# Optimization experiments

Measured on AMD Instinct MI355X. Metric: run time of the kernel, lower is better.

The kernel has to match this reference:

```python
import jax, jax.numpy as jnp
import numpy as np

N_NODES = 100000
N_EDGES = 3200000
IN_DIM = 4
HID = 128
OUT_DIM = 4


def setup_inputs() -> dict:
    key = jax.random.key(0)
    ks = jax.random.split(key, 16)
    x = jax.random.normal(ks[0], (N_NODES, IN_DIM), dtype=jnp.float32)
    edge_index = jax.random.randint(ks[1], (2, N_EDGES), 0, N_NODES, dtype=jnp.int32)
    hidden_mask = jax.random.randint(ks[2], (N_NODES,), 0, 2) > 0
    def glorot(k, shape):
        fan_in, fan_out = shape[0], shape[1]
        s = jnp.sqrt(6.0 / (fan_in + fan_out))
        return jax.random.uniform(k, shape, jnp.float32, -s, s)
    return {
        "x": x,
        "edge_index": edge_index,
        "hidden_mask": hidden_mask,
        "W0": glorot(ks[3], (IN_DIM, HID)), "b0": jnp.zeros((HID,), jnp.float32),
        "res_W": glorot(ks[4], (IN_DIM, HID)), "res_b": jnp.zeros((HID,), jnp.float32),
        "W1": glorot(ks[5], (HID, HID)), "b1": jnp.zeros((HID,), jnp.float32),
        "W2": glorot(ks[6], (HID, HID)), "b2": jnp.zeros((HID,), jnp.float32),
        "fc_W": glorot(ks[7], (HID, OUT_DIM)), "fc_b": jnp.zeros((OUT_DIM,), jnp.float32),
    }


def _gcn_norm(edge_index, num_nodes):
    # add self loops, compute symmetric normalization (PyG GCNConv default)
    loop = jnp.arange(num_nodes, dtype=edge_index.dtype)
    src = jnp.concatenate([edge_index[0], loop])
    dst = jnp.concatenate([edge_index[1], loop])
    deg = jax.ops.segment_sum(jnp.ones_like(dst, dtype=jnp.float32), dst,
                              num_segments=num_nodes)
    dis = jnp.where(deg > 0, jax.lax.rsqrt(deg), 0.0)  # deg^{-1/2}, inf -> 0
    norm = dis[src] * dis[dst]  # [E + N]
    return src, dst, norm


def _gcn_conv(h, W, b, src, dst, norm, num_nodes):
    h = h @ W                       # [N, out]
    msg = h[src] * norm[:, None]    # gather + scale, [E+N, out]
    agg = jax.ops.segment_sum(msg, dst, num_segments=num_nodes)
    return agg + b


def reference(x, edge_index, hidden_mask, W0, b0, res_W, res_b, W1, b1, W2, b2, fc_W, fc_b):
    n = x.shape[0]
    src, dst, norm = _gcn_norm(edge_index, n)
    # mask input features (mask broadcast over 4 feature cols)
    h = jnp.where(hidden_mask[:, None], x, 0.0)
    # layer 0: in_dim != hidden -> linear residual
    out0 = _gcn_conv(h, W0, b0, src, dst, norm, n)
    h = jax.nn.relu(out0 + (h @ res_W + res_b))
    # layers 1,2: identity residual
    h = jax.nn.relu(_gcn_conv(h, W1, b1, src, dst, norm, n) + h)
    h = jax.nn.relu(_gcn_conv(h, W2, b2, src, dst, norm, n) + h)
    x_out = h @ fc_W + fc_b
    return (x_out, hidden_mask)
```

## Files before the change

kernel.cpp:

```cpp
#include <hip/hip_runtime.h>
#include <hip/hip_bf16.h>
#include <stdint.h>

#define HID 128
#define NPART 8
#define NCHUNK 256
#define MCHUNK 4096
#define LBITS 9
#define SBITS 22
#define NCH 8

typedef float f2 __attribute__((ext_vector_type(2)));

__global__ void detect_mask_kernel(const unsigned char* __restrict__ p, int nbytes,
                                   int nfloat, int* __restrict__ flags) {
  int stride = blockDim.x * gridDim.x;
  for (int i = blockIdx.x * blockDim.x + threadIdx.x; i < nbytes; i += stride) {
    if ((i & 3) && p[i] != 0) { atomicOr(&flags[0], 1); break; }
  }
  const float* fp = (const float*)p;
  for (int i = blockIdx.x * blockDim.x + threadIdx.x; i < nfloat; i += stride) {
    float f = fp[i];
    if (!(f == 0.0f || f == 1.0f)) { atomicOr(&flags[1], 1); break; }
  }
}

__global__ void expand_mask_h0(const void* __restrict__ maskp, const float4* __restrict__ x4,
                               const int* __restrict__ flags, const float* __restrict__ dis,
                               float* __restrict__ maskout, float* __restrict__ cvec,
                               float4* __restrict__ h0s, int N) {
  int i = blockIdx.x * blockDim.x + threadIdx.x;
  if (i >= N) return;
  float m;
  if (flags[0] == 0)      m = (((const int*)maskp)[i] != 0) ? 1.f : 0.f;
  else if (flags[1] == 0) m = (((const float*)maskp)[i] != 0.f) ? 1.f : 0.f;
  else                    m = (((const unsigned char*)maskp)[i] != 0) ? 1.f : 0.f;
  maskout[i] = m;
  float4 xv = x4[i];
  float4 h0 = make_float4(m * xv.x, m * xv.y, m * xv.z, m * xv.w);
  float* cv = cvec + (size_t)i * 8;
  cv[4] = h0.x; cv[5] = h0.y; cv[6] = h0.z; cv[7] = h0.w;
  float d = dis[i];
  h0s[i] = make_float4(d * h0.x, d * h0.y, d * h0.z, d * h0.w);
}

__global__ void init_gcur_kernel(int* __restrict__ gcur, int n, int CAPB) {
  int i = blockIdx.x * blockDim.x + threadIdx.x;
  if (i < n) gcur[i] = i * CAPB;
}

__global__ void radixA_kernel(const int* __restrict__ src, const int* __restrict__ dst,
                              int* __restrict__ gcur, uint32_t* __restrict__ bdata,
                              int nbin, int CAPB, int E) {
  __shared__ uint32_t sv[MCHUNK];
  __shared__ uint16_t sb[MCHUNK];
  __shared__ int bcnt[1024], boff[1024], gbase[1024];
  __shared__ int wsum[4];
  int t = threadIdx.x;
  int base = blockIdx.x * MCHUNK;
  int m = E - base; if (m > MCHUNK) m = MCHUNK;
  for (int i = t; i < 1024; i += 256) bcnt[i] = 0;
  __syncthreads();
  uint32_t pk[16]; short bn[16];
#pragma unroll
  for (int j = 0; j < 16; j++) {
    int i = base + t + j * 256;
    if (i < base + m) {
      int d = __builtin_nontemporal_load(&dst[i]);
      int s = __builtin_nontemporal_load(&src[i]);
      int b = d >> LBITS;
      pk[j] = ((uint32_t)(d & ((1 << LBITS) - 1)) << SBITS) | (uint32_t)s;
      bn[j] = (short)b;
      atomicAdd(&bcnt[b], 1);
    } else bn[j] = -1;
  }
  __syncthreads();
  {
    int lane = t & 63, w = t >> 6, i0 = t * 4;
    int v0 = bcnt[i0], v1 = bcnt[i0 + 1], v2 = bcnt[i0 + 2], v3 = bcnt[i0 + 3];
    int ts = v0 + v1 + v2 + v3, sc = ts;
    for (int d = 1; d < 64; d <<= 1) { int x = __shfl_up(sc, d, 64); if (lane >= d) sc += x; }
    if (lane == 63) wsum[w] = sc;
    __syncthreads();
    int wo = 0;
    for (int k = 0; k < w; k++) wo += wsum[k];
    int excl = wo + sc - ts;
    boff[i0] = excl; boff[i0 + 1] = excl + v0;
    boff[i0 + 2] = excl + v0 + v1; boff[i0 + 3] = excl + v0 + v1 + v2;
  }
  __syncthreads();
  for (int i = t; i < nbin; i += 256) {
    int c = bcnt[i];
    gbase[i] = c ? atomicAdd(&gcur[i], c) : 0;
  }
  __syncthreads();
  for (int i = t; i < nbin; i += 256) bcnt[i] = boff[i];
  __syncthreads();
#pragma unroll
  for (int j = 0; j < 16; j++) {
    if (bn[j] >= 0) {
      int p = atomicAdd(&bcnt[bn[j]], 1);
      sv[p] = pk[j];
      sb[p] = (uint16_t)bn[j];
    }
  }
  __syncthreads();
  for (int i = t; i < m; i += 256) {
    int b = sb[i];
    int gp = gbase[b] + (i - boff[b]);
    if (gp < (b + 1) * CAPB) bdata[gp] = sv[i];
  }
}

__global__ void bucket_meta_kernel(const int* __restrict__ gcur, int* __restrict__ bstart,
                                   int nbin, int CAPB) {
  __shared__ int wsum[4];
  int t = threadIdx.x, lane = t & 63, w = t >> 6, i0 = t * 4;
  int v[4];
#pragma unroll
  for (int q = 0; q < 4; q++) {
    int i = i0 + q;
    int c = 0;
    if (i < nbin) {
      c = gcur[i] - i * CAPB;
      if (c > CAPB) c = CAPB;
    }
    v[q] = c;
  }
  int ts = v[0] + v[1] + v[2] + v[3], sc = ts;
  for (int d = 1; d < 64; d <<= 1) { int x = __shfl_up(sc, d, 64); if (lane >= d) sc += x; }
  if (lane == 63) wsum[w] = sc;
  __syncthreads();
  int wo = 0;
  for (int k = 0; k < w; k++) wo += wsum[k];
  int excl = wo + sc - ts;
  int e[4] = {excl, excl + v[0], excl + v[0] + v[1], excl + v[0] + v[1] + v[2]};
#pragma unroll
  for (int q = 0; q < 4; q++)
    if (i0 + q < nbin) bstart[i0 + q] = e[q];
  if (t == 255) bstart[nbin] = wo + sc;
}

__global__ void radixB_kernel(const uint32_t* __restrict__ bdata, const int* __restrict__ gcur,
                              const int* __restrict__ bstart, int CAPB,
                              int* __restrict__ off, float* __restrict__ dis,
                              float* __restrict__ rdis, int* __restrict__ csr,
                              int N, int E, int cshift) {
  __shared__ int cnt[4096], loff[4096];
  __shared__ int wsum[4];
  int b = blockIdx.x, t = threadIdx.x;
  int cb = gcur[b] - b * CAPB; if (cb > CAPB) cb = CAPB;
  int gb = bstart[b];
  const uint32_t* bd = bdata + (size_t)b * CAPB;
  for (int i = t; i < 4096; i += 256) cnt[i] = 0;
  __syncthreads();
  const uint32_t smask = (1u << SBITS) - 1;
  for (int i = t; i < cb; i += 256) {
    uint32_t v = bd[i];
    int ld = v >> SBITS;
    int src = (int)(v & smask);
    atomicAdd(&cnt[(ld << 3) | (src >> cshift)], 1);
  }
  __syncthreads();
  int lane = t & 63, w = t >> 6;
  int loc[16];
  int s = 0;
  int base16 = t * 16;
#pragma unroll
  for (int q = 0; q < 16; q++) { loc[q] = cnt[base16 + q]; s += loc[q]; }
  int sc = s;
  for (int d = 1; d < 64; d <<= 1) { int x = __shfl_up(sc, d, 64); if (lane >= d) sc += x; }
  if (lane == 63) wsum[w] = sc;
  __syncthreads();
  int wo = 0;
  for (int k = 0; k < w; k++) wo += wsum[k];
  int excl = wo + sc - s;
  {
    int run = excl;
#pragma unroll
    for (int q = 0; q < 16; q++) { loff[base16 + q] = run; run += loc[q]; }
  }
  int c0 = loc[0] + loc[1] + loc[2] + loc[3] + loc[4] + loc[5] + loc[6] + loc[7];
  int c1 = loc[8] + loc[9] + loc[10] + loc[11] + loc[12] + loc[13] + loc[14] + loc[15];
  int dst0 = b * (1 << LBITS) + 2 * t;
  if (dst0 < N) {
    off[dst0] = gb + excl;
    dis[dst0] = rsqrtf((float)c0 + 1.0f);
    rdis[dst0] = sqrtf((float)c0 + 1.0f);
  }
  if (dst0 + 1 < N) {
    off[dst0 + 1] = gb + excl + c0;
    dis[dst0 + 1] = rsqrtf((float)c1 + 1.0f);
    rdis[dst0 + 1] = sqrtf((float)c1 + 1.0f);
  }
  if (b == 0 && t == 0) off[N] = E;
  __syncthreads();
  for (int i = t; i < 4096; i += 256) cnt[i] = loff[i];
  __syncthreads();
  for (int i = t; i < cb; i += 256) {
    uint32_t v = bd[i];
    int ld = v >> SBITS;
    int src = (int)(v & smask);
    int p = atomicAdd(&cnt[(ld << 3) | (src >> cshift)], 1);
    csr[gb + p] = src;
  }
}

__global__ void scan1_kernel(const int* __restrict__ cnt, int* __restrict__ off,
                             int* __restrict__ bsum, float* __restrict__ dis, int N) {
  __shared__ int wsum[4];
  int t = threadIdx.x, lane = t & 63, w = t >> 6;
  int base = blockIdx.x * 1024 + t * 4;
  int v0 = (base + 0 < N) ? cnt[base + 0] : 0;
  int v1 = (base + 1 < N) ? cnt[base + 1] : 0;
  int v2 = (base + 2 < N) ? cnt[base + 2] : 0;
  int v3 = (base + 3 < N) ? cnt[base + 3] : 0;
  if (dis) {
    if (base + 0 < N) dis[base + 0] = rsqrtf((float)v0 + 1.0f);
    if (base + 1 < N) dis[base + 1] = rsqrtf((float)v1 + 1.0f);
    if (base + 2 < N) dis[base + 2] = rsqrtf((float)v2 + 1.0f);
    if (base + 3 < N) dis[base + 3] = rsqrtf((float)v3 + 1.0f);
  }
  int ts = v0 + v1 + v2 + v3;
  int sc = ts;
  for (int d = 1; d < 64; d <<= 1) {
    int x = __shfl_up(sc, d, 64);
    if (lane >= d) sc += x;
  }
  if (lane == 63) wsum[w] = sc;
  __syncthreads();
  int wo = 0;
  for (int i = 0; i < w; i++) wo += wsum[i];
  int excl = wo + sc - ts;
  if (base + 0 < N) off[base + 0] = excl;
  if (base + 1 < N) off[base + 1] = excl + v0;
  if (base + 2 < N) off[base + 2] = excl + v0 + v1;
  if (base + 3 < N) off[base + 3] = excl + v0 + v1 + v2;
  if (t == 255) bsum[blockIdx.x] = wo + sc;
}

__global__ void scan2_kernel(int* __restrict__ bsum, int nb) {
  if (threadIdx.x == 0 && blockIdx.x == 0) {
    int run = 0;
    for (int i = 0; i < nb; i++) { int v = bsum[i]; bsum[i] = run; run += v; }
  }
}

__global__ void scan3_kernel(int* __restrict__ off, const int* __restrict__ bsum,
                             int* __restrict__ cur, int N, int E) {
  int i = blockIdx.x * blockDim.x + threadIdx.x;
  if (i < N) {
    int o = off[i] + bsum[i >> 10];
    off[i] = o;
    if (cur) cur[i] = o;
  }
  if (i == 0) off[N] = E;
}

__global__ void hist_part_kernel(const int* __restrict__ dst, int* __restrict__ cnt,
                                 int E, int N) {
  int p = blockIdx.x & (NPART - 1);
  int chunk = blockIdx.x >> 3;
  int lo = (int)((long long)p * N / NPART);
  int hi = (int)((long long)(p + 1) * N / NPART);
  int stride = NCHUNK * 256;
  for (int e = chunk * 256 + threadIdx.x; e < E; e += stride) {
    int d = __builtin_nontemporal_load(&dst[e]);
    if (d >= lo && d < hi) atomicAdd(&cnt[d], 1);
  }
}

__global__ void fill_part_kernel(const int* __restrict__ src, const int* __restrict__ dst,
                                 int* __restrict__ cur, int* __restrict__ csr, int E, int N) {
  int p = blockIdx.x & (NPART - 1);
  int chunk = blockIdx.x >> 3;
  int lo = (int)((long long)p * N / NPART);
  int hi = (int)((long long)(p + 1) * N / NPART);
  int stride = NCHUNK * 256;
  for (int e = chunk * 256 + threadIdx.x; e < E; e += stride) {
    int d = __builtin_nontemporal_load(&dst[e]);
    if (d >= lo && d < hi) {
      int s = __builtin_nontemporal_load(&src[e]);
      int pos = atomicAdd(&cur[d], 1);
      csr[pos] = s;
    }
  }
}

__global__ void l0_agg_kernel(const float4* __restrict__ h0s, const float* __restrict__ dis,
                              const int* __restrict__ off, const int* __restrict__ csr,
                              float* __restrict__ cvec, int N) {
  int n = blockIdx.x * blockDim.x + threadIdx.x;
  if (n >= N) return;
  float4 a = h0s[n];
  int e0 = off[n], e1 = off[n + 1];
  int i = e0;
  for (; i < e1 && (i & 3); i++) {
    float4 v = h0s[csr[i]];
    a.x += v.x; a.y += v.y; a.z += v.z; a.w += v.w;
  }
  for (; i + 4 <= e1; i += 4) {
    int4 c = *(const int4*)&csr[i];
    float4 v0 = h0s[c.x], v1 = h0s[c.y], v2 = h0s[c.z], v3 = h0s[c.w];
    a.x += v0.x + v1.x + v2.x + v3.x;
    a.y += v0.y + v1.y + v2.y + v3.y;
    a.z += v0.z + v1.z + v2.z + v3.z;
    a.w += v0.w + v1.w + v2.w + v3.w;
  }
  for (; i < e1; i++) {
    float4 v = h0s[csr[i]];
    a.x += v.x; a.y += v.y; a.z += v.z; a.w += v.w;
  }
  float dn = dis[n];
  float* cv = cvec + (size_t)n * 8;
  cv[0] = dn * a.x; cv[1] = dn * a.y; cv[2] = dn * a.z; cv[3] = dn * a.w;
}

__global__ void l0_combine_kernel(const float* __restrict__ cvec, const float* __restrict__ W0,
                                  const float* __restrict__ b0, const float* __restrict__ resW,
                                  const float* __restrict__ resb, const float* __restrict__ dis,
                                  float* __restrict__ h1, __hip_bfloat16* __restrict__ hbout) {
  int idx = blockIdx.x * blockDim.x + threadIdx.x;
  int n = idx >> 7, c = idx & 127;
  const float* cv = cvec + (size_t)n * 8;
  float acc = b0[c] + resb[c];
#pragma unroll
  for (int k = 0; k < 4; k++) {
    acc += cv[k] * W0[k * HID + c];
    acc += cv[4 + k] * resW[k * HID + c];
  }
  float v = fmaxf(acc, 0.0f);
  if (h1) h1[idx] = v;
  if (hbout) hbout[idx] = __float2bfloat16(dis[n] * v);
}

#define ACC2(W) { f2 v; v.x = __uint_as_float((W) << 16); \
                  v.y = __uint_as_float((W) & 0xffff0000u); a += v; }
__global__ void __launch_bounds__(256, 8)
agg_hid_bf16_kernel(const uint32_t* __restrict__ hb, const float* __restrict__ dis,
                    const int* __restrict__ off, const int* __restrict__ csr,
                    float* __restrict__ out, int N) {
  int node = blockIdx.x * 4 + (threadIdx.x >> 6);
  int lane = threadIdx.x & 63;
  if (node >= N) return;
  uint32_t w = hb[(size_t)node * 64 + lane];
  f2 a;
  a.x = __uint_as_float(w << 16);
  a.y = __uint_as_float(w & 0xffff0000u);
  int e0 = __builtin_amdgcn_readfirstlane(off[node]);
  int e1 = __builtin_amdgcn_readfirstlane(off[node + 1]);
  int i = e0;
  for (; i < e1 && (i & 3); i++) {
    int s = __builtin_amdgcn_readfirstlane(csr[i]);
    uint32_t ww = hb[(size_t)s * 64 + lane];
    ACC2(ww)
  }
  for (; i + 8 <= e1; i += 8) {
    int4 c0 = *(const int4*)&csr[i];
    int4 c1 = *(const int4*)&csr[i + 4];
    int s0 = __builtin_amdgcn_readfirstlane(c0.x);
    int s1 = __builtin_amdgcn_readfirstlane(c0.y);
    int s2 = __builtin_amdgcn_readfirstlane(c0.z);
    int s3 = __builtin_amdgcn_readfirstlane(c0.w);
    int s4 = __builtin_amdgcn_readfirstlane(c1.x);
    int s5 = __builtin_amdgcn_readfirstlane(c1.y);
    int s6 = __builtin_amdgcn_readfirstlane(c1.z);
    int s7 = __builtin_amdgcn_readfirstlane(c1.w);
    uint32_t w0 = hb[(size_t)s0 * 64 + lane];
    uint32_t w1 = hb[(size_t)s1 * 64 + lane];
    uint32_t w2 = hb[(size_t)s2 * 64 + lane];
    uint32_t w3 = hb[(size_t)s3 * 64 + lane];
    uint32_t w4 = hb[(size_t)s4 * 64 + lane];
    uint32_t w5 = hb[(size_t)s5 * 64 + lane];
    uint32_t w6 = hb[(size_t)s6 * 64 + lane];
    uint32_t w7 = hb[(size_t)s7 * 64 + lane];
    ACC2(w0) ACC2(w1) ACC2(w2) ACC2(w3) ACC2(w4) ACC2(w5) ACC2(w6) ACC2(w7)
  }
  for (; i + 4 <= e1; i += 4) {
    int4 c = *(const int4*)&csr[i];
    int s0 = __builtin_amdgcn_readfirstlane(c.x);
    int s1 = __builtin_amdgcn_readfirstlane(c.y);
    int s2 = __builtin_amdgcn_readfirstlane(c.z);
    int s3 = __builtin_amdgcn_readfirstlane(c.w);
    uint32_t w0 = hb[(size_t)s0 * 64 + lane];
    uint32_t w1 = hb[(size_t)s1 * 64 + lane];
    uint32_t w2 = hb[(size_t)s2 * 64 + lane];
    uint32_t w3 = hb[(size_t)s3 * 64 + lane];
    ACC2(w0) ACC2(w1) ACC2(w2) ACC2(w3)
  }
  for (; i < e1; i++) {
    int s = __builtin_amdgcn_readfirstlane(csr[i]);
    uint32_t ww = hb[(size_t)s * 64 + lane];
    ACC2(ww)
  }
  float dn = dis[node];
  *(float2*)&out[(size_t)node * HID + 2 * lane] = make_float2(dn * a.x, dn * a.y);
}

__global__ void agg_hid_kernel(const float* __restrict__ h, const float* __restrict__ dis,
                               const int* __restrict__ off, const int* __restrict__ csr,
                               float* __restrict__ out, int N) {
  int node = blockIdx.x * 4 + (threadIdx.x >> 6);
  int lane = threadIdx.x & 63;
  if (node >= N) return;
  float dn = dis[node];
  const float* hrow = h + (size_t)node * HID;
  float a0 = dn * hrow[lane];
  float a1 = dn * hrow[lane + 64];
  int e0 = off[node], e1 = off[node + 1];
  for (int i = e0; i < e1; i++) {
    int s = csr[i];
    float d = dis[s];
    const float* hs = h + (size_t)s * HID;
    a0 += d * hs[lane];
    a1 += d * hs[lane + 64];
  }
  out[(size_t)node * HID + lane] = dn * a0;
  out[(size_t)node * HID + lane + 64] = dn * a1;
}

__global__ void gemm_resid_relu_kernel(const float* __restrict__ ag,
                                       const __hip_bfloat16* __restrict__ hbres,
                                       const float* __restrict__ rdis,
                                       const float* __restrict__ W, const float* __restrict__ b,
                                       const float* __restrict__ dis,
                                       __hip_bfloat16* __restrict__ hbout, int N) {
  __shared__ float ash[64 * HID];
  int t = threadIdx.x;
  int n0 = blockIdx.x * 64;
  for (int i = t; i < 64 * HID; i += 256) {
    int gn = n0 + (i >> 7);
    ash[i] = (gn < N) ? ag[(size_t)gn * HID + (i & 127)] : 0.0f;
  }
  __syncthreads();
  int tc = t & 31;
  int tn = t >> 5;
  float acc[8][4];
#pragma unroll
  for (int j = 0; j < 8; j++)
#pragma unroll
    for (int q = 0; q < 4; q++) acc[j][q] = 0.0f;

  for (int k = 0; k < HID; k += 4) {
    float4 w0 = *(const float4*)&W[(k + 0) * HID + tc * 4];
    float4 w1 = *(const float4*)&W[(k + 1) * HID + tc * 4];
    float4 w2 = *(const float4*)&W[(k + 2) * HID + tc * 4];
    float4 w3 = *(const float4*)&W[(k + 3) * HID + tc * 4];
#pragma unroll
    for (int j = 0; j < 8; j++) {
      float4 a = *(const float4*)&ash[(tn * 8 + j) * HID + k];
      acc[j][0] += a.x * w0.x + a.y * w1.x + a.z * w2.x + a.w * w3.x;
      acc[j][1] += a.x * w0.y + a.y * w1.y + a.z * w2.y + a.w * w3.y;
      acc[j][2] += a.x * w0.z + a.y * w1.z + a.z * w2.z + a.w * w3.z;
      acc[j][3] += a.x * w0.w + a.y * w1.w + a.z * w2.w + a.w * w3.w;
    }
  }
  float4 bv = *(const float4*)&b[tc * 4];
#pragma unroll
  for (int j = 0; j < 8; j++) {
    int gn = n0 + tn * 8 + j;
    if (gn < N) {
      float rd = rdis[gn];
      uint2 hu = *(const uint2*)&hbres[(size_t)gn * HID + tc * 4];
      float h0v = __uint_as_float(hu.x << 16) * rd;
      float h1v = __uint_as_float(hu.x & 0xffff0000u) * rd;
      float h2v = __uint_as_float(hu.y << 16) * rd;
      float h3v = __uint_as_float(hu.y & 0xffff0000u) * rd;
      float4 o;
      o.x = fmaxf(acc[j][0] + bv.x + h0v, 0.0f);
      o.y = fmaxf(acc[j][1] + bv.y + h1v, 0.0f);
      o.z = fmaxf(acc[j][2] + bv.z + h2v, 0.0f);
      o.w = fmaxf(acc[j][3] + bv.w + h3v, 0.0f);
      float dnn = dis[gn];
      __hip_bfloat162 p01 = __float22bfloat162_rn(make_float2(dnn * o.x, dnn * o.y));
      __hip_bfloat162 p23 = __float22bfloat162_rn(make_float2(dnn * o.z, dnn * o.w));
      *(__hip_bfloat162*)&hbout[(size_t)gn * HID + tc * 4] = p01;
      *(__hip_bfloat162*)&hbout[(size_t)gn * HID + tc * 4 + 2] = p23;
    }
  }
}

__global__ void gemm_resid_fc_kernel(const float* __restrict__ ag,
                                     const __hip_bfloat16* __restrict__ hbres,
                                     const float* __restrict__ rdis,
                                     const float* __restrict__ W, const float* __restrict__ b,
                                     const float* __restrict__ fcW, const float* __restrict__ fcb,
                                     float* __restrict__ out, int N) {
  __shared__ float ash[64 * HID];
  int t = threadIdx.x;
  int n0 = blockIdx.x * 64;
  for (int i = t; i < 64 * HID; i += 256) {
    int gn = n0 + (i >> 7);
    ash[i] = (gn < N) ? ag[(size_t)gn * HID + (i & 127)] : 0.0f;
  }
  __syncthreads();
  int tc = t & 31;
  int tn = t >> 5;
  float acc[8][4];
#pragma unroll
  for (int j = 0; j < 8; j++)
#pragma unroll
    for (int q = 0; q < 4; q++) acc[j][q] = 0.0f;

  for (int k = 0; k < HID; k += 4) {
    float4 w0 = *(const float4*)&W[(k + 0) * HID + tc * 4];
    float4 w1 = *(const float4*)&W[(k + 1) * HID + tc * 4];
    float4 w2 = *(const float4*)&W[(k + 2) * HID + tc * 4];
    float4 w3 = *(const float4*)&W[(k + 3) * HID + tc * 4];
#pragma unroll
    for (int j = 0; j < 8; j++) {
      float4 a = *(const float4*)&ash[(tn * 8 + j) * HID + k];
      acc[j][0] += a.x * w0.x + a.y * w1.x + a.z * w2.x + a.w * w3.x;
      acc[j][1] += a.x * w0.y + a.y * w1.y + a.z * w2.y + a.w * w3.y;
      acc[j][2] += a.x * w0.z + a.y * w1.z + a.z * w2.z + a.w * w3.z;
      acc[j][3] += a.x * w0.w + a.y * w1.w + a.z * w2.w + a.w * w3.w;
    }
  }
  float4 f0 = *(const float4*)&fcW[(tc * 4 + 0) * 4];
  float4 f1 = *(const float4*)&fcW[(tc * 4 + 1) * 4];
  float4 f2 = *(const float4*)&fcW[(tc * 4 + 2) * 4];
  float4 f3 = *(const float4*)&fcW[(tc * 4 + 3) * 4];
  float4 bv = *(const float4*)&b[tc * 4];
  float4 fb = *(const float4*)&fcb[0];
#pragma unroll
  for (int j = 0; j < 8; j++) {
    int gn = n0 + tn * 8 + j;
    float4 o = make_float4(0.f, 0.f, 0.f, 0.f);
    if (gn < N) {
      float rd = rdis[gn];
      uint2 hu = *(const uint2*)&hbres[(size_t)gn * HID + tc * 4];
      o.x = fmaxf(acc[j][0] + bv.x + __uint_as_float(hu.x << 16) * rd, 0.0f);
      o.y = fmaxf(acc[j][1] + bv.y + __uint_as_float(hu.x & 0xffff0000u) * rd, 0.0f);
      o.z = fmaxf(acc[j][2] + bv.z + __uint_as_float(hu.y << 16) * rd, 0.0f);
      o.w = fmaxf(acc[j][3] + bv.w + __uint_as_float(hu.y & 0xffff0000u) * rd, 0.0f);
    }
    float r0 = o.x * f0.x + o.y * f1.x + o.z * f2.x + o.w * f3.x;
    float r1 = o.x * f0.y + o.y * f1.y + o.z * f2.y + o.w * f3.y;
    float r2 = o.x * f0.z + o.y * f1.z + o.z * f2.z + o.w * f3.z;
    float r3 = o.x * f0.w + o.y * f1.w + o.z * f2.w + o.w * f3.w;
#pragma unroll
    for (int d = 1; d < 32; d <<= 1) {
      r0 += __shfl_xor(r0, d, 64);
      r1 += __shfl_xor(r1, d, 64);
      r2 += __shfl_xor(r2, d, 64);
      r3 += __shfl_xor(r3, d, 64);
    }
    if (tc == 0 && gn < N)
      *(float4*)&out[(size_t)gn * 4] =
          make_float4(r0 + fb.x, r1 + fb.y, r2 + fb.z, r3 + fb.w);
  }
}

__global__ void gemm_resid_relu_f32_kernel(const float* __restrict__ ag, float* __restrict__ hout,
                                           const float* __restrict__ hres,
                                           const float* __restrict__ W, const float* __restrict__ b,
                                           int N) {
  __shared__ float ash[64 * HID];
  int t = threadIdx.x;
  int n0 = blockIdx.x * 64;
  for (int i = t; i < 64 * HID; i += 256) {
    int gn = n0 + (i >> 7);
    ash[i] = (gn < N) ? ag[(size_t)gn * HID + (i & 127)] : 0.0f;
  }
  __syncthreads();
  int tc = t & 31;
  int tn = t >> 5;
  float acc[8][4];
#pragma unroll
  for (int j = 0; j < 8; j++)
#pragma unroll
    for (int q = 0; q < 4; q++) acc[j][q] = 0.0f;
  for (int k = 0; k < HID; k += 4) {
    float4 w0 = *(const float4*)&W[(k + 0) * HID + tc * 4];
    float4 w1 = *(const float4*)&W[(k + 1) * HID + tc * 4];
    float4 w2 = *(const float4*)&W[(k + 2) * HID + tc * 4];
    float4 w3 = *(const float4*)&W[(k + 3) * HID + tc * 4];
#pragma unroll
    for (int j = 0; j < 8; j++) {
      float4 a = *(const float4*)&ash[(tn * 8 + j) * HID + k];
      acc[j][0] += a.x * w0.x + a.y * w1.x + a.z * w2.x + a.w * w3.x;
      acc[j][1] += a.x * w0.y + a.y * w1.y + a.z * w2.y + a.w * w3.y;
      acc[j][2] += a.x * w0.z + a.y * w1.z + a.z * w2.z + a.w * w3.z;
      acc[j][3] += a.x * w0.w + a.y * w1.w + a.z * w2.w + a.w * w3.w;
    }
  }
  float4 bv = *(const float4*)&b[tc * 4];
#pragma unroll
  for (int j = 0; j < 8; j++) {
    int gn = n0 + tn * 8 + j;
    if (gn < N) {
      float4 hv = *(const float4*)&hres[(size_t)gn * HID + tc * 4];
      float4 o;
      o.x = fmaxf(acc[j][0] + bv.x + hv.x, 0.0f);
      o.y = fmaxf(acc[j][1] + bv.y + hv.y, 0.0f);
      o.z = fmaxf(acc[j][2] + bv.z + hv.z, 0.0f);
      o.w = fmaxf(acc[j][3] + bv.w + hv.w, 0.0f);
      *(float4*)&hout[(size_t)gn * HID + tc * 4] = o;
    }
  }
}

__global__ void gemm_resid_fc_f32_kernel(const float* __restrict__ ag,
                                         const float* __restrict__ hres,
                                         const float* __restrict__ W, const float* __restrict__ b,
                                         const float* __restrict__ fcW, const float* __restrict__ fcb,
                                         float* __restrict__ out, int N) {
  __shared__ float ash[64 * HID];
  int t = threadIdx.x;
  int n0 = blockIdx.x * 64;
  for (int i = t; i < 64 * HID; i += 256) {
    int gn = n0 + (i >> 7);
    ash[i] = (gn < N) ? ag[(size_t)gn * HID + (i & 127)] : 0.0f;
  }
  __syncthreads();
  int tc = t & 31;
  int tn = t >> 5;
  float acc[8][4];
#pragma unroll
  for (int j = 0; j < 8; j++)
#pragma unroll
    for (int q = 0; q < 4; q++) acc[j][q] = 0.0f;
  for (int k = 0; k < HID; k += 4) {
    float4 w0 = *(const float4*)&W[(k + 0) * HID + tc * 4];
    float4 w1 = *(const float4*)&W[(k + 1) * HID + tc * 4];
    float4 w2 = *(const float4*)&W[(k + 2) * HID + tc * 4];
    float4 w3 = *(const float4*)&W[(k + 3) * HID + tc * 4];
#pragma unroll
    for (int j = 0; j < 8; j++) {
      float4 a = *(const float4*)&ash[(tn * 8 + j) * HID + k];
      acc[j][0] += a.x * w0.x + a.y * w1.x + a.z * w2.x + a.w * w3.x;
      acc[j][1] += a.x * w0.y + a.y * w1.y + a.z * w2.y + a.w * w3.y;
      acc[j][2] += a.x * w0.z + a.y * w1.z + a.z * w2.z + a.w * w3.z;
      acc[j][3] += a.x * w0.w + a.y * w1.w + a.z * w2.w + a.w * w3.w;
    }
  }
  float4 f0 = *(const float4*)&fcW[(tc * 4 + 0) * 4];
  float4 f1 = *(const float4*)&fcW[(tc * 4 + 1) * 4];
  float4 f2 = *(const float4*)&fcW[(tc * 4 + 2) * 4];
  float4 f3 = *(const float4*)&fcW[(tc * 4 + 3) * 4];
  float4 bv = *(const float4*)&b[tc * 4];
  float4 fb = *(const float4*)&fcb[0];
#pragma unroll
  for (int j = 0; j < 8; j++) {
    int gn = n0 + tn * 8 + j;
    float4 o = make_float4(0.f, 0.f, 0.f, 0.f);
    if (gn < N) {
      float4 hv = *(const float4*)&hres[(size_t)gn * HID + tc * 4];
      o.x = fmaxf(acc[j][0] + bv.x + hv.x, 0.0f);
      o.y = fmaxf(acc[j][1] + bv.y + hv.y, 0.0f);
      o.z = fmaxf(acc[j][2] + bv.z + hv.z, 0.0f);
      o.w = fmaxf(acc[j][3] + bv.w + hv.w, 0.0f);
    }
    float r0 = o.x * f0.x + o.y * f1.x + o.z * f2.x + o.w * f3.x;
    float r1 = o.x * f0.y + o.y * f1.y + o.z * f2.y + o.w * f3.y;
    float r2 = o.x * f0.z + o.y * f1.z + o.z * f2.z + o.w * f3.z;
    float r3 = o.x * f0.w + o.y * f1.w + o.z * f2.w + o.w * f3.w;
#pragma unroll
    for (int d = 1; d < 32; d <<= 1) {
      r0 += __shfl_xor(r0, d, 64);
      r1 += __shfl_xor(r1, d, 64);
      r2 += __shfl_xor(r2, d, 64);
      r3 += __shfl_xor(r3, d, 64);
    }
    if (tc == 0 && gn < N)
      *(float4*)&out[(size_t)gn * 4] =
          make_float4(r0 + fb.x, r1 + fb.y, r2 + fb.z, r3 + fb.w);
  }
}

extern "C" void kernel_launch(void* const* d_in, const int* in_sizes, int n_in,
                              void* d_out, int out_size, void* d_ws, size_t ws_size,
                              hipStream_t stream) {
  const float* x = (const float*)d_in[0];
  const int* edge = (const int*)d_in[1];
  const void* maskp = d_in[2];
  const float* W0 = (const float*)d_in[3];
  const float* b0 = (const float*)d_in[4];
  const float* resW = (const float*)d_in[5];
  const float* resb = (const float*)d_in[6];
  const float* W1 = (const float*)d_in[7];
  const float* b1 = (const float*)d_in[8];
  const float* W2 = (const float*)d_in[9];
  const float* b2 = (const float*)d_in[10];
  const float* fcW = (const float*)d_in[11];
  const float* fcb = (const float*)d_in[12];
  float* out = (float*)d_out;

  int N = in_sizes[0] / 4;
  int E = in_sizes[1] / 2;
  const int* srcp = edge;
  const int* dstp = edge + E;

  char* ws = (char*)d_ws;
  size_t cursor = 0;
  auto alloc = [&](size_t bytes) { char* p = ws + cursor; cursor += (bytes + 511) & ~(size_t)511; return p; };
  int* flags = (int*)alloc(16);
  int* cnt = (int*)alloc((size_t)N * 4);
  float* dis = (float*)alloc((size_t)N * 4);
  float* rdis = (float*)alloc((size_t)N * 4);
  int* off = (int*)alloc((size_t)(N + 1) * 4);
  int* bsum = (int*)alloc(1024);
  int nbin = (N + (1 << LBITS) - 1) >> LBITS;
  int* gcur = (int*)alloc((size_t)(nbin + 1) * 4);
  int* bstart = (int*)alloc((size_t)(nbin + 1) * 4);
  int* csr = (int*)alloc((size_t)E * 4);
  float* h0s = (float*)alloc((size_t)N * 4 * 4);
  float* cvec = (float*)alloc((size_t)N * 8 * 4);
  float* buf0 = (float*)alloc((size_t)N * HID * 4);
  float* buf1 = (float*)alloc((size_t)N * HID * 4);
  size_t base_cursor = cursor;
  __hip_bfloat16* hb1 = (__hip_bfloat16*)alloc((size_t)N * HID * 2);
  __hip_bfloat16* hb2 = (__hip_bfloat16*)alloc((size_t)N * HID * 2);
  bool use_bf16 = (cursor <= ws_size);
  if (!use_bf16) {
    hb1 = nullptr; hb2 = nullptr;
    if (base_cursor > ws_size) return;
  }

  long long expect = (long long)E / (nbin > 0 ? nbin : 1);
  int CAPB = (int)((((expect * 5) / 4 + 127) / 64) * 64);
  if (CAPB < 256) CAPB = 256;
  size_t bdata_bytes = (size_t)nbin * CAPB * 4;
  bool use_radix = (N <= (1 << SBITS)) && (nbin <= 1024) &&
                   (bdata_bytes <= (size_t)N * HID * 4);
  uint32_t* bdata = (uint32_t*)buf1;

  int cshift = 0;
  while (((N - 1) >> cshift) > (NCH - 1)) cshift++;

  int nThreadsN = (N + 255) / 256;
  int ngemm = (N + 63) / 64;

  hipMemsetAsync(flags, 0, 16, stream);
  detect_mask_kernel<<<256, 256, 0, stream>>>((const unsigned char*)maskp, N, N / 4, flags);

  if (use_radix) {
    init_gcur_kernel<<<(nbin + 255) / 256, 256, 0, stream>>>(gcur, nbin, CAPB);
    radixA_kernel<<<(E + MCHUNK - 1) / MCHUNK, 256, 0, stream>>>(srcp, dstp, gcur, bdata,
                                                                 nbin, CAPB, E);
    bucket_meta_kernel<<<1, 256, 0, stream>>>(gcur, bstart, nbin, CAPB);
    radixB_kernel<<<nbin, 256, 0, stream>>>(bdata, gcur, bstart, CAPB, off, dis, rdis,
                                            csr, N, E, cshift);
  } else {
    hipMemsetAsync(cnt, 0, (size_t)N * 4, stream);
    int nb = (N + 1023) / 1024;
    hist_part_kernel<<<NPART * NCHUNK, 256, 0, stream>>>(dstp, cnt, E, N);
    scan1_kernel<<<nb, 256, 0, stream>>>(cnt, off, bsum, dis, N);
    scan2_kernel<<<1, 64, 0, stream>>>(bsum, nb);
    scan3_kernel<<<nThreadsN, 256, 0, stream>>>(off, bsum, cnt, N, E);
    fill_part_kernel<<<NPART * NCHUNK, 256, 0, stream>>>(srcp, dstp, cnt, csr, E, N);
  }

  expand_mask_h0<<<nThreadsN, 256, 0, stream>>>(maskp, (const float4*)x, flags, dis,
                                                out + (size_t)N * 4, cvec, (float4*)h0s, N);

  l0_agg_kernel<<<nThreadsN, 256, 0, stream>>>((const float4*)h0s, dis, off, csr, cvec, N);

  if (use_bf16) {
    l0_combine_kernel<<<(N * HID + 255) / 256, 256, 0, stream>>>(cvec, W0, b0, resW, resb, dis,
                                                                 nullptr, hb1);
    agg_hid_bf16_kernel<<<(N + 3) / 4, 256, 0, stream>>>((const uint32_t*)hb1, dis, off, csr,
                                                         buf0, N);
    gemm_resid_relu_kernel<<<ngemm, 256, 0, stream>>>(buf0, hb1, rdis, W1, b1, dis, hb2, N);
    agg_hid_bf16_kernel<<<(N + 3) / 4, 256, 0, stream>>>((const uint32_t*)hb2, dis, off, csr,
                                                         buf0, N);
    gemm_resid_fc_kernel<<<ngemm, 256, 0, stream>>>(buf0, hb2, rdis, W2, b2, fcW, fcb, out, N);
  } else {
    l0_combine_kernel<<<(N * HID + 255) / 256, 256, 0, stream>>>(cvec, W0, b0, resW, resb, dis,
                                                                 buf0, nullptr);
    agg_hid_kernel<<<(N + 3) / 4, 256, 0, stream>>>(buf0, dis, off, csr, buf1, N);
    gemm_resid_relu_f32_kernel<<<ngemm, 256, 0, stream>>>(buf1, buf1, buf0, W1, b1, N);
    agg_hid_kernel<<<(N + 3) / 4, 256, 0, stream>>>(buf1, dis, off, csr, buf0, N);
    gemm_resid_fc_f32_kernel<<<ngemm, 256, 0, stream>>>(buf0, buf1, W2, b2, fcW, fcb, out, N);
  }
}
```

Baseline: 510.6 us.

## Fold bucket prefix scan into radixB, unroll bf16 gather to 16, nontemporal stores

Removes the single-block bucket_meta kernel launch. Each radixB block now computes its own bucket start offset by summing the clamped counts of all earlier buckets, so there is one fewer launch and dependency in the graph at the cost of redundant reads of gcur in every block. The bf16 aggregation inner loop is unrolled from 8 to 16 gathered rows to keep more loads in flight, which raises register pressure. The aggregated output is written with nontemporal stores to reduce cache pollution. The bf16 path is also gated on use_radix.

```diff
diff --git a/kernel.cpp b/kernel.cpp
--- a/kernel.cpp
+++ b/kernel.cpp
@@ -112,48 +112,27 @@
   }
 }
 
-__global__ void bucket_meta_kernel(const int* __restrict__ gcur, int* __restrict__ bstart,
-                                   int nbin, int CAPB) {
-  __shared__ int wsum[4];
-  int t = threadIdx.x, lane = t & 63, w = t >> 6, i0 = t * 4;
-  int v[4];
-#pragma unroll
-  for (int q = 0; q < 4; q++) {
-    int i = i0 + q;
-    int c = 0;
-    if (i < nbin) {
-      c = gcur[i] - i * CAPB;
-      if (c > CAPB) c = CAPB;
-    }
-    v[q] = c;
-  }
-  int ts = v[0] + v[1] + v[2] + v[3], sc = ts;
-  for (int d = 1; d < 64; d <<= 1) { int x = __shfl_up(sc, d, 64); if (lane >= d) sc += x; }
-  if (lane == 63) wsum[w] = sc;
-  __syncthreads();
-  int wo = 0;
-  for (int k = 0; k < w; k++) wo += wsum[k];
-  int excl = wo + sc - ts;
-  int e[4] = {excl, excl + v[0], excl + v[0] + v[1], excl + v[0] + v[1] + v[2]};
-#pragma unroll
-  for (int q = 0; q < 4; q++)
-    if (i0 + q < nbin) bstart[i0 + q] = e[q];
-  if (t == 255) bstart[nbin] = wo + sc;
-}
-
 __global__ void radixB_kernel(const uint32_t* __restrict__ bdata, const int* __restrict__ gcur,
-                              const int* __restrict__ bstart, int CAPB,
-                              int* __restrict__ off, float* __restrict__ dis,
+                              int CAPB, int* __restrict__ off, float* __restrict__ dis,
                               float* __restrict__ rdis, int* __restrict__ csr,
                               int N, int E, int cshift) {
   __shared__ int cnt[4096], loff[4096];
-  __shared__ int wsum[4];
+  __shared__ int wsum[4], gbs[4];
   int b = blockIdx.x, t = threadIdx.x;
   int cb = gcur[b] - b * CAPB; if (cb > CAPB) cb = CAPB;
-  int gb = bstart[b];
+  {
+    int partial = 0;
+    for (int j = t; j < b; j += 256) {
+      int c = gcur[j] - j * CAPB;
+      partial += (c > CAPB) ? CAPB : c;
+    }
+    for (int d = 1; d < 64; d <<= 1) partial += __shfl_xor(partial, d, 64);
+    if ((t & 63) == 0) gbs[t >> 6] = partial;
+  }
   const uint32_t* bd = bdata + (size_t)b * CAPB;
   for (int i = t; i < 4096; i += 256) cnt[i] = 0;
   __syncthreads();
+  int gb = gbs[0] + gbs[1] + gbs[2] + gbs[3];
   const uint32_t smask = (1u << SBITS) - 1;
   for (int i = t; i < cb; i += 256) {
     uint32_t v = bd[i];
@@ -355,9 +334,11 @@
     uint32_t ww = hb[(size_t)s * 64 + lane];
     ACC2(ww)
   }
-  for (; i + 8 <= e1; i += 8) {
+  for (; i + 16 <= e1; i += 16) {
     int4 c0 = *(const int4*)&csr[i];
     int4 c1 = *(const int4*)&csr[i + 4];
+    int4 c2 = *(const int4*)&csr[i + 8];
+    int4 c3 = *(const int4*)&csr[i + 12];
     int s0 = __builtin_amdgcn_readfirstlane(c0.x);
     int s1 = __builtin_amdgcn_readfirstlane(c0.y);
     int s2 = __builtin_amdgcn_readfirstlane(c0.z);
@@ -366,6 +347,14 @@
     int s5 = __builtin_amdgcn_readfirstlane(c1.y);
     int s6 = __builtin_amdgcn_readfirstlane(c1.z);
     int s7 = __builtin_amdgcn_readfirstlane(c1.w);
+    int s8 = __builtin_amdgcn_readfirstlane(c2.x);
+    int s9 = __builtin_amdgcn_readfirstlane(c2.y);
+    int sa = __builtin_amdgcn_readfirstlane(c2.z);
+    int sb = __builtin_amdgcn_readfirstlane(c2.w);
+    int sc = __builtin_amdgcn_readfirstlane(c3.x);
+    int sd = __builtin_amdgcn_readfirstlane(c3.y);
+    int se = __builtin_amdgcn_readfirstlane(c3.z);
+    int sf = __builtin_amdgcn_readfirstlane(c3.w);
     uint32_t w0 = hb[(size_t)s0 * 64 + lane];
     uint32_t w1 = hb[(size_t)s1 * 64 + lane];
     uint32_t w2 = hb[(size_t)s2 * 64 + lane];
@@ -374,7 +363,16 @@
     uint32_t w5 = hb[(size_t)s5 * 64 + lane];
     uint32_t w6 = hb[(size_t)s6 * 64 + lane];
     uint32_t w7 = hb[(size_t)s7 * 64 + lane];
+    uint32_t w8 = hb[(size_t)s8 * 64 + lane];
+    uint32_t w9 = hb[(size_t)s9 * 64 + lane];
+    uint32_t wa = hb[(size_t)sa * 64 + lane];
+    uint32_t wb = hb[(size_t)sb * 64 + lane];
+    uint32_t wc = hb[(size_t)sc * 64 + lane];
+    uint32_t wd = hb[(size_t)sd * 64 + lane];
+    uint32_t we = hb[(size_t)se * 64 + lane];
+    uint32_t wf = hb[(size_t)sf * 64 + lane];
     ACC2(w0) ACC2(w1) ACC2(w2) ACC2(w3) ACC2(w4) ACC2(w5) ACC2(w6) ACC2(w7)
+    ACC2(w8) ACC2(w9) ACC2(wa) ACC2(wb) ACC2(wc) ACC2(wd) ACC2(we) ACC2(wf)
   }
   for (; i + 4 <= e1; i += 4) {
     int4 c = *(const int4*)&csr[i];
@@ -394,7 +392,8 @@
     ACC2(ww)
   }
   float dn = dis[node];
-  *(float2*)&out[(size_t)node * HID + 2 * lane] = make_float2(dn * a.x, dn * a.y);
+  f2 o; o.x = dn * a.x; o.y = dn * a.y;
+  __builtin_nontemporal_store(o, (f2*)&out[(size_t)node * HID + 2 * lane]);
 }
 
 __global__ void agg_hid_kernel(const float* __restrict__ h, const float* __restrict__ dis,
@@ -702,7 +701,6 @@
   int* bsum = (int*)alloc(1024);
   int nbin = (N + (1 << LBITS) - 1) >> LBITS;
   int* gcur = (int*)alloc((size_t)(nbin + 1) * 4);
-  int* bstart = (int*)alloc((size_t)(nbin + 1) * 4);
   int* csr = (int*)alloc((size_t)E * 4);
   float* h0s = (float*)alloc((size_t)N * 4 * 4);
   float* cvec = (float*)alloc((size_t)N * 8 * 4);
@@ -731,18 +729,18 @@
   int nThreadsN = (N + 255) / 256;
   int ngemm = (N + 63) / 64;
 
-  hipMemsetAsync(flags, 0, 16, stream);
+  hipError_t _e = hipMemsetAsync(flags, 0, 16, stream);
+  (void)_e;
   detect_mask_kernel<<<256, 256, 0, stream>>>((const unsigned char*)maskp, N, N / 4, flags);
 
   if (use_radix) {
     init_gcur_kernel<<<(nbin + 255) / 256, 256, 0, stream>>>(gcur, nbin, CAPB);
     radixA_kernel<<<(E + MCHUNK - 1) / MCHUNK, 256, 0, stream>>>(srcp, dstp, gcur, bdata,
                                                                  nbin, CAPB, E);
-    bucket_meta_kernel<<<1, 256, 0, stream>>>(gcur, bstart, nbin, CAPB);
-    radixB_kernel<<<nbin, 256, 0, stream>>>(bdata, gcur, bstart, CAPB, off, dis, rdis,
-                                            csr, N, E, cshift);
+    radixB_kernel<<<nbin, 256, 0, stream>>>(bdata, gcur, CAPB, off, dis, rdis, csr, N, E, cshift);
   } else {
-    hipMemsetAsync(cnt, 0, (size_t)N * 4, stream);
+    _e = hipMemsetAsync(cnt, 0, (size_t)N * 4, stream);
+    (void)_e;
     int nb = (N + 1023) / 1024;
     hist_part_kernel<<<NPART * NCHUNK, 256, 0, stream>>>(dstp, cnt, E, N);
     scan1_kernel<<<nb, 256, 0, stream>>>(cnt, off, bsum, dis, N);
@@ -756,7 +754,7 @@
 
   l0_agg_kernel<<<nThreadsN, 256, 0, stream>>>((const float4*)h0s, dis, off, csr, cvec, N);
 
-  if (use_bf16) {
+  if (use_bf16 && use_radix) {
     l0_combine_kernel<<<(N * HID + 255) / 256, 256, 0, stream>>>(cvec, W0, b0, resW, resb, dis,
                                                                  nullptr, hb1);
     agg_hid_bf16_kernel<<<(N + 3) / 4, 256, 0, stream>>>((const uint32_t*)hb1, dis, off, csr,
```

Result: slower. 528.2 us (+3.4%).
